# Kernel tuning notes

Measured on AMD Instinct MI355X. Metric: run time of the kernel, lower is better.

## Reference

```python
import jax, jax.numpy as jnp
import numpy as np

N_EMBED = 1024
HEAD_SIZE = 64
BLOCK_SIZE = 2048


def setup_inputs() -> dict:
    key = jax.random.key(0)
    kx, kk, kv = jax.random.split(key, 3)
    x = jax.random.normal(kx, (8, 2048, N_EMBED), dtype=jnp.float32)
    # nn.Linear(n_embed, head_size, bias=False): weight [head_size, n_embed]
    scale = 1.0 / np.sqrt(N_EMBED)
    W_k = jax.random.uniform(kk, (HEAD_SIZE, N_EMBED), dtype=jnp.float32, minval=-scale, maxval=scale)
    W_v = jax.random.uniform(kv, (HEAD_SIZE, N_EMBED), dtype=jnp.float32, minval=-scale, maxval=scale)
    return {"x": x, "W_k": W_k, "W_v": W_v}


def reference(x, W_k, W_v):
    # Faithful to source: q = self.key(x) (query projection is unused in the original forward)
    T = x.shape[1]
    k = jnp.einsum('btc,hc->bth', x, W_k)   # [B,T,H]
    q = k                                    # source bug: q uses key projection
    wei = jnp.einsum('bth,bsh->bts', q, k) * (HEAD_SIZE ** -0.5)  # [B,T,T]
    causal = jnp.tril(jnp.ones((T, T), dtype=bool))
    wei = jnp.where(causal, wei, -jnp.inf)
    wei = jax.nn.softmax(wei, axis=-1)
    v = jnp.einsum('btc,hc->bth', x, W_v)
    out = jnp.einsum('bts,bsh->bth', wei, v)
    return out
```

## Files before the change

kernel.cpp:

```cpp
#include <hip/hip_runtime.h>


typedef __bf16 bf16;
typedef __bf16 bf16x4 __attribute__((ext_vector_type(4)));
typedef __bf16 bf16x8 __attribute__((ext_vector_type(8)));
typedef float  floatx4 __attribute__((ext_vector_type(4)));

#define T_LEN 2048
#define HEAD  64
#define CEMB  1024

static __device__ __forceinline__ bf16x8 cvt2(float4 a, float4 b) {
    bf16x8 r;
    r[0] = (bf16)a.x; r[1] = (bf16)a.y; r[2] = (bf16)a.z; r[3] = (bf16)a.w;
    r[4] = (bf16)b.x; r[5] = (bf16)b.y; r[6] = (bf16)b.z; r[7] = (bf16)b.w;
    return r;
}

__global__ __launch_bounds__(256) void proj_kernel(const float* __restrict__ x,
                                                   const float* __restrict__ Wk,
                                                   const float* __restrict__ Wv,
                                                   bf16* __restrict__ Kbuf,
                                                   bf16* __restrict__ Vt) {
    __shared__ __align__(16) bf16 As[64][72];
    __shared__ __align__(16) bf16 Bs[128][72];

    const int tid  = threadIdx.x;
    const int wave = tid >> 6;
    const int lane = tid & 63;
    const int quad = lane >> 4;
    const int low  = lane & 15;

    const long row0 = (long)blockIdx.x * 64;

    const int a_row = tid >> 2;
    const int a_col = (tid & 3) * 16;
    const int b_row = tid >> 1;
    const int b_col = (tid & 1) * 32;

    const float* abase = x + (row0 + a_row) * CEMB + a_col;
    const float* wrow  = ((b_row < 64) ? (Wk + b_row * CEMB) : (Wv + (b_row - 64) * CEMB)) + b_col;

    floatx4 acc[8];
#pragma unroll
    for (int i = 0; i < 8; ++i) acc[i] = (floatx4){0.f, 0.f, 0.f, 0.f};

    float4 apf[4], bpf[8];
#pragma unroll
    for (int i = 0; i < 4; ++i) apf[i] = ((const float4*)abase)[i];
#pragma unroll
    for (int i = 0; i < 8; ++i) bpf[i] = ((const float4*)wrow)[i];

    for (int s = 0; s < 16; ++s) {
        __syncthreads();
        *(bf16x8*)&As[a_row][a_col]     = cvt2(apf[0], apf[1]);
        *(bf16x8*)&As[a_row][a_col + 8] = cvt2(apf[2], apf[3]);
#pragma unroll
        for (int i = 0; i < 4; ++i)
            *(bf16x8*)&Bs[b_row][b_col + 8 * i] = cvt2(bpf[2 * i], bpf[2 * i + 1]);

        if (s < 15) {
            const int k0 = (s + 1) * 64;
#pragma unroll
            for (int i = 0; i < 4; ++i) apf[i] = ((const float4*)(abase + k0))[i];
#pragma unroll
            for (int i = 0; i < 8; ++i) bpf[i] = ((const float4*)(wrow + k0))[i];
        }
        __syncthreads();

#pragma unroll
        for (int h = 0; h < 2; ++h) {
            bf16x8 afrag = *(const bf16x8*)&As[wave * 16 + low][h * 32 + quad * 8];
#pragma unroll
            for (int nt = 0; nt < 8; ++nt) {
                bf16x8 bfrag = *(const bf16x8*)&Bs[nt * 16 + low][h * 32 + quad * 8];
                acc[nt] = __builtin_amdgcn_mfma_f32_16x16x32_bf16(afrag, bfrag, acc[nt], 0, 0, 0);
            }
        }
    }

    const long b     = row0 >> 11;
    const int  tloc0 = (int)(row0 & 2047);
#pragma unroll
    for (int nt = 0; nt < 8; ++nt) {
#pragma unroll
        for (int r = 0; r < 4; ++r) {
            int trow = tloc0 + wave * 16 + quad * 4 + r;
            int c    = nt * 16 + low;
            bf16 val = (bf16)acc[nt][r];
            if (c < HEAD) {
                Kbuf[(b * T_LEN + trow) * HEAD + c] = val;
            } else {
                Vt[(b * HEAD + (c - HEAD)) * T_LEN + trow] = val;
            }
        }
    }
}

__global__ __launch_bounds__(256) void attn_kernel(const bf16* __restrict__ Kbuf,
                                                   const bf16* __restrict__ Vt,
                                                   float* __restrict__ out) {
    __shared__ __align__(16) bf16 Qs[64][72];
    __shared__ __align__(16) bf16 Ks[64][72];
    __shared__ __align__(16) bf16 Vs[64][72];
    __shared__ __align__(16) bf16 Ps[64][72];

    const int tid  = threadIdx.x;
    const int wave = tid >> 6;
    const int lane = tid & 63;
    const int quad = lane >> 4;
    const int low  = lane & 15;

    const int b  = blockIdx.x >> 5;
    const int qb = blockIdx.x & 31;

    const bf16* kbase = Kbuf + (long)b * T_LEN * HEAD;
    const bf16* vbase = Vt + (long)b * HEAD * T_LEN;

    const int s_row = tid >> 2;
    const int s_col = (tid & 3) * 16;

    {
        const bf16* src = kbase + (qb * 64 + s_row) * HEAD + s_col;
        *(float4*)&Qs[s_row][s_col]     = *(const float4*)(src);
        *(float4*)&Qs[s_row][s_col + 8] = *(const float4*)(src + 8);
    }
    __syncthreads();
    const bf16x8 qf0 = *(const bf16x8*)&Qs[wave * 16 + low][quad * 8];
    const bf16x8 qf1 = *(const bf16x8*)&Qs[wave * 16 + low][32 + quad * 8];

    bf16x8 ones;
#pragma unroll
    for (int i = 0; i < 8; ++i) ones[i] = (bf16)1.0f;

    floatx4 o[4], ol;
#pragma unroll
    for (int nt = 0; nt < 4; ++nt) o[nt] = (floatx4){0.f, 0.f, 0.f, 0.f};
    ol = (floatx4){0.f, 0.f, 0.f, 0.f};

    const bf16* ksrc = kbase + s_row * HEAD + s_col;
    const bf16* vsrc = vbase + (long)s_row * T_LEN + s_col;

    float4 kpf0 = *(const float4*)(ksrc);
    float4 kpf1 = *(const float4*)(ksrc + 8);
    float4 vpf0 = *(const float4*)(vsrc);
    float4 vpf1 = *(const float4*)(vsrc + 8);

    for (int j = 0; j <= qb; ++j) {
        __syncthreads();
        *(float4*)&Ks[s_row][s_col]     = kpf0;
        *(float4*)&Ks[s_row][s_col + 8] = kpf1;
        *(float4*)&Vs[s_row][s_col]     = vpf0;
        *(float4*)&Vs[s_row][s_col + 8] = vpf1;
        if (j < qb) {
            kpf0 = *(const float4*)(ksrc + (j + 1) * 4096);
            kpf1 = *(const float4*)(ksrc + (j + 1) * 4096 + 8);
            vpf0 = *(const float4*)(vsrc + (j + 1) * 64);
            vpf1 = *(const float4*)(vsrc + (j + 1) * 64 + 8);
        }
        __syncthreads();

        floatx4 s_[4];
#pragma unroll
        for (int nt = 0; nt < 4; ++nt) {
            bf16x8 kf0 = *(const bf16x8*)&Ks[nt * 16 + low][quad * 8];
            bf16x8 kf1 = *(const bf16x8*)&Ks[nt * 16 + low][32 + quad * 8];
            floatx4 z = (floatx4){0.f, 0.f, 0.f, 0.f};
            z = __builtin_amdgcn_mfma_f32_16x16x32_bf16(qf0, kf0, z, 0, 0, 0);
            z = __builtin_amdgcn_mfma_f32_16x16x32_bf16(qf1, kf1, z, 0, 0, 0);
            s_[nt] = z;
        }

        const bool diag = (j == qb);
#pragma unroll
        for (int nt = 0; nt < 4; ++nt) {
#pragma unroll
            for (int r = 0; r < 4; ++r) {
                float p = __builtin_amdgcn_exp2f(s_[nt][r] * 0.180336880f);
                if (diag && (nt * 16 + low) > (wave * 16 + quad * 4 + r)) p = 0.f;
                Ps[wave * 16 + quad * 4 + r][nt * 16 + low] = (bf16)p;
            }
        }

        bf16x8 pf0 = *(const bf16x8*)&Ps[wave * 16 + low][quad * 8];
        bf16x8 pf1 = *(const bf16x8*)&Ps[wave * 16 + low][32 + quad * 8];
#pragma unroll
        for (int nt = 0; nt < 4; ++nt) {
            bf16x8 vf0 = *(const bf16x8*)&Vs[nt * 16 + low][quad * 8];
            bf16x8 vf1 = *(const bf16x8*)&Vs[nt * 16 + low][32 + quad * 8];
            o[nt] = __builtin_amdgcn_mfma_f32_16x16x32_bf16(pf0, vf0, o[nt], 0, 0, 0);
            o[nt] = __builtin_amdgcn_mfma_f32_16x16x32_bf16(pf1, vf1, o[nt], 0, 0, 0);
        }
        ol = __builtin_amdgcn_mfma_f32_16x16x32_bf16(pf0, ones, ol, 0, 0, 0);
        ol = __builtin_amdgcn_mfma_f32_16x16x32_bf16(pf1, ones, ol, 0, 0, 0);
    }

#pragma unroll
    for (int nt = 0; nt < 4; ++nt) {
#pragma unroll
        for (int r = 0; r < 4; ++r) {
            int trow = qb * 64 + wave * 16 + quad * 4 + r;
            int h    = nt * 16 + low;
            out[((long)b * T_LEN + trow) * HEAD + h] = o[nt][r] / ol[r];
        }
    }
}

extern "C" void kernel_launch(void* const* d_in, const int* in_sizes, int n_in,
                              void* d_out, int out_size, void* d_ws, size_t ws_size,
                              hipStream_t stream) {
    const float* x  = (const float*)d_in[0];
    const float* Wk = (const float*)d_in[1];
    const float* Wv = (const float*)d_in[2];
    float* out = (float*)d_out;

    char* ws = (char*)d_ws;
    bf16* Kbuf = (bf16*)ws;
    bf16* Vt   = (bf16*)(ws + (2 << 20));

    proj_kernel<<<256, 256, 0, stream>>>(x, Wk, Wv, Kbuf, Vt);
    attn_kernel<<<256, 256, 0, stream>>>(Kbuf, Vt, out);
}
```

Baseline: 142.2 us.

## Split attention KV range across blocks and retile projection for more parallelism

The projection kernel now uses 32-row tiles, with each block computing either K or V, so it launches four times as many blocks. The attention kernel splits the causal KV loop of each query tile into four interleaved chunks, one per block, and writes unnormalized partial outputs and row sums to workspace. A new combine kernel sums the four partials and normalizes them. The aim is to fill the 256-CU device and reduce causal load imbalance, at the cost of an extra launch, partial-result traffic, and reloading the Q tile in every block.

```diff
diff --git a/kernel.cpp b/kernel.cpp
--- a/kernel.cpp
+++ b/kernel.cpp
@@ -2,7 +2,6 @@
 
 
 typedef __bf16 bf16;
-typedef __bf16 bf16x4 __attribute__((ext_vector_type(4)));
 typedef __bf16 bf16x8 __attribute__((ext_vector_type(8)));
 typedef float  floatx4 __attribute__((ext_vector_type(4)));
 
@@ -22,8 +21,8 @@
                                                    const float* __restrict__ Wv,
                                                    bf16* __restrict__ Kbuf,
                                                    bf16* __restrict__ Vt) {
-    __shared__ __align__(16) bf16 As[64][72];
-    __shared__ __align__(16) bf16 Bs[128][72];
+    __shared__ __align__(16) bf16 As[32][72];
+    __shared__ __align__(16) bf16 Bs[64][72];
 
     const int tid  = threadIdx.x;
     const int wave = tid >> 6;
@@ -31,75 +30,75 @@
     const int quad = lane >> 4;
     const int low  = lane & 15;
 
-    const long row0 = (long)blockIdx.x * 64;
-
-    const int a_row = tid >> 2;
-    const int a_col = (tid & 3) * 16;
-    const int b_row = tid >> 1;
-    const int b_col = (tid & 1) * 32;
+    const int mblk  = blockIdx.x >> 1;
+    const int nhalf = blockIdx.x & 1;
+    const long row0 = (long)mblk * 32;
+
+    const int a_row = tid >> 3;
+    const int a_col = (tid & 7) * 8;
+    const int b_row = tid >> 2;
+    const int b_col = (tid & 3) * 16;
 
     const float* abase = x + (row0 + a_row) * CEMB + a_col;
-    const float* wrow  = ((b_row < 64) ? (Wk + b_row * CEMB) : (Wv + (b_row - 64) * CEMB)) + b_col;
-
-    floatx4 acc[8];
-#pragma unroll
-    for (int i = 0; i < 8; ++i) acc[i] = (floatx4){0.f, 0.f, 0.f, 0.f};
-
-    float4 apf[4], bpf[8];
-#pragma unroll
-    for (int i = 0; i < 4; ++i) apf[i] = ((const float4*)abase)[i];
-#pragma unroll
-    for (int i = 0; i < 8; ++i) bpf[i] = ((const float4*)wrow)[i];
+    const float* wrow  = (nhalf ? Wv : Wk) + b_row * CEMB + b_col;
+
+    const int strip = wave & 1;
+    const int npair = wave >> 1;
+
+    floatx4 acc[2];
+    acc[0] = (floatx4){0.f, 0.f, 0.f, 0.f};
+    acc[1] = (floatx4){0.f, 0.f, 0.f, 0.f};
+
+    float4 apf[2], bpf[4];
+#pragma unroll
+    for (int i = 0; i < 2; ++i) apf[i] = ((const float4*)abase)[i];
+#pragma unroll
+    for (int i = 0; i < 4; ++i) bpf[i] = ((const float4*)wrow)[i];
 
     for (int s = 0; s < 16; ++s) {
         __syncthreads();
-        *(bf16x8*)&As[a_row][a_col]     = cvt2(apf[0], apf[1]);
-        *(bf16x8*)&As[a_row][a_col + 8] = cvt2(apf[2], apf[3]);
-#pragma unroll
-        for (int i = 0; i < 4; ++i)
-            *(bf16x8*)&Bs[b_row][b_col + 8 * i] = cvt2(bpf[2 * i], bpf[2 * i + 1]);
-
+        *(bf16x8*)&As[a_row][a_col] = cvt2(apf[0], apf[1]);
+        *(bf16x8*)&Bs[b_row][b_col]     = cvt2(bpf[0], bpf[1]);
+        *(bf16x8*)&Bs[b_row][b_col + 8] = cvt2(bpf[2], bpf[3]);
         if (s < 15) {
             const int k0 = (s + 1) * 64;
 #pragma unroll
-            for (int i = 0; i < 4; ++i) apf[i] = ((const float4*)(abase + k0))[i];
-#pragma unroll
-            for (int i = 0; i < 8; ++i) bpf[i] = ((const float4*)(wrow + k0))[i];
+            for (int i = 0; i < 2; ++i) apf[i] = ((const float4*)(abase + k0))[i];
+#pragma unroll
+            for (int i = 0; i < 4; ++i) bpf[i] = ((const float4*)(wrow + k0))[i];
         }
         __syncthreads();
 
 #pragma unroll
         for (int h = 0; h < 2; ++h) {
-            bf16x8 afrag = *(const bf16x8*)&As[wave * 16 + low][h * 32 + quad * 8];
-#pragma unroll
-            for (int nt = 0; nt < 8; ++nt) {
-                bf16x8 bfrag = *(const bf16x8*)&Bs[nt * 16 + low][h * 32 + quad * 8];
-                acc[nt] = __builtin_amdgcn_mfma_f32_16x16x32_bf16(afrag, bfrag, acc[nt], 0, 0, 0);
-            }
-        }
-    }
-
-    const long b     = row0 >> 11;
-    const int  tloc0 = (int)(row0 & 2047);
-#pragma unroll
-    for (int nt = 0; nt < 8; ++nt) {
+            bf16x8 afrag = *(const bf16x8*)&As[strip * 16 + low][h * 32 + quad * 8];
+#pragma unroll
+            for (int i = 0; i < 2; ++i) {
+                bf16x8 bfrag = *(const bf16x8*)&Bs[(npair * 2 + i) * 16 + low][h * 32 + quad * 8];
+                acc[i] = __builtin_amdgcn_mfma_f32_16x16x32_bf16(afrag, bfrag, acc[i], 0, 0, 0);
+            }
+        }
+    }
+
+#pragma unroll
+    for (int i = 0; i < 2; ++i) {
 #pragma unroll
         for (int r = 0; r < 4; ++r) {
-            int trow = tloc0 + wave * 16 + quad * 4 + r;
-            int c    = nt * 16 + low;
-            bf16 val = (bf16)acc[nt][r];
-            if (c < HEAD) {
-                Kbuf[(b * T_LEN + trow) * HEAD + c] = val;
-            } else {
-                Vt[(b * HEAD + (c - HEAD)) * T_LEN + trow] = val;
-            }
+            long trow = row0 + strip * 16 + quad * 4 + r;
+            long b    = trow >> 11;
+            int  tloc = (int)(trow & 2047);
+            int  cl   = (npair * 2 + i) * 16 + low;
+            bf16 val  = (bf16)acc[i][r];
+            if (nhalf == 0) Kbuf[(b * T_LEN + tloc) * HEAD + cl] = val;
+            else            Vt[(b * HEAD + cl) * T_LEN + tloc]   = val;
         }
     }
 }
 
 __global__ __launch_bounds__(256) void attn_kernel(const bf16* __restrict__ Kbuf,
                                                    const bf16* __restrict__ Vt,
-                                                   float* __restrict__ out) {
+                                                   float* __restrict__ Opart,
+                                                   float* __restrict__ lpart) {
     __shared__ __align__(16) bf16 Qs[64][72];
     __shared__ __align__(16) bf16 Ks[64][72];
     __shared__ __align__(16) bf16 Vs[64][72];
@@ -111,8 +110,9 @@
     const int quad = lane >> 4;
     const int low  = lane & 15;
 
-    const int b  = blockIdx.x >> 5;
-    const int qb = blockIdx.x & 31;
+    const int c  = blockIdx.x & 3;
+    const int qb = (blockIdx.x >> 2) & 31;
+    const int b  = blockIdx.x >> 7;
 
     const bf16* kbase = Kbuf + (long)b * T_LEN * HEAD;
     const bf16* vbase = Vt + (long)b * HEAD * T_LEN;
@@ -141,69 +141,109 @@
     const bf16* ksrc = kbase + s_row * HEAD + s_col;
     const bf16* vsrc = vbase + (long)s_row * T_LEN + s_col;
 
-    float4 kpf0 = *(const float4*)(ksrc);
-    float4 kpf1 = *(const float4*)(ksrc + 8);
-    float4 vpf0 = *(const float4*)(vsrc);
-    float4 vpf1 = *(const float4*)(vsrc + 8);
-
-    for (int j = 0; j <= qb; ++j) {
-        __syncthreads();
-        *(float4*)&Ks[s_row][s_col]     = kpf0;
-        *(float4*)&Ks[s_row][s_col + 8] = kpf1;
-        *(float4*)&Vs[s_row][s_col]     = vpf0;
-        *(float4*)&Vs[s_row][s_col + 8] = vpf1;
-        if (j < qb) {
-            kpf0 = *(const float4*)(ksrc + (j + 1) * 4096);
-            kpf1 = *(const float4*)(ksrc + (j + 1) * 4096 + 8);
-            vpf0 = *(const float4*)(vsrc + (j + 1) * 64);
-            vpf1 = *(const float4*)(vsrc + (j + 1) * 64 + 8);
-        }
-        __syncthreads();
-
-        floatx4 s_[4];
-#pragma unroll
-        for (int nt = 0; nt < 4; ++nt) {
-            bf16x8 kf0 = *(const bf16x8*)&Ks[nt * 16 + low][quad * 8];
-            bf16x8 kf1 = *(const bf16x8*)&Ks[nt * 16 + low][32 + quad * 8];
-            floatx4 z = (floatx4){0.f, 0.f, 0.f, 0.f};
-            z = __builtin_amdgcn_mfma_f32_16x16x32_bf16(qf0, kf0, z, 0, 0, 0);
-            z = __builtin_amdgcn_mfma_f32_16x16x32_bf16(qf1, kf1, z, 0, 0, 0);
-            s_[nt] = z;
-        }
-
-        const bool diag = (j == qb);
-#pragma unroll
-        for (int nt = 0; nt < 4; ++nt) {
-#pragma unroll
-            for (int r = 0; r < 4; ++r) {
-                float p = __builtin_amdgcn_exp2f(s_[nt][r] * 0.180336880f);
-                if (diag && (nt * 16 + low) > (wave * 16 + quad * 4 + r)) p = 0.f;
-                Ps[wave * 16 + quad * 4 + r][nt * 16 + low] = (bf16)p;
-            }
-        }
-
-        bf16x8 pf0 = *(const bf16x8*)&Ps[wave * 16 + low][quad * 8];
-        bf16x8 pf1 = *(const bf16x8*)&Ps[wave * 16 + low][32 + quad * 8];
-#pragma unroll
-        for (int nt = 0; nt < 4; ++nt) {
-            bf16x8 vf0 = *(const bf16x8*)&Vs[nt * 16 + low][quad * 8];
-            bf16x8 vf1 = *(const bf16x8*)&Vs[nt * 16 + low][32 + quad * 8];
-            o[nt] = __builtin_amdgcn_mfma_f32_16x16x32_bf16(pf0, vf0, o[nt], 0, 0, 0);
-            o[nt] = __builtin_amdgcn_mfma_f32_16x16x32_bf16(pf1, vf1, o[nt], 0, 0, 0);
-        }
-        ol = __builtin_amdgcn_mfma_f32_16x16x32_bf16(pf0, ones, ol, 0, 0, 0);
-        ol = __builtin_amdgcn_mfma_f32_16x16x32_bf16(pf1, ones, ol, 0, 0, 0);
-    }
-
+    if (c <= qb) {
+        float4 kpf0 = *(const float4*)(ksrc + c * 4096);
+        float4 kpf1 = *(const float4*)(ksrc + c * 4096 + 8);
+        float4 vpf0 = *(const float4*)(vsrc + c * 64);
+        float4 vpf1 = *(const float4*)(vsrc + c * 64 + 8);
+
+        for (int j = c; j <= qb; j += 4) {
+            __syncthreads();
+            *(float4*)&Ks[s_row][s_col]     = kpf0;
+            *(float4*)&Ks[s_row][s_col + 8] = kpf1;
+            *(float4*)&Vs[s_row][s_col]     = vpf0;
+            *(float4*)&Vs[s_row][s_col + 8] = vpf1;
+            if (j + 4 <= qb) {
+                kpf0 = *(const float4*)(ksrc + (j + 4) * 4096);
+                kpf1 = *(const float4*)(ksrc + (j + 4) * 4096 + 8);
+                vpf0 = *(const float4*)(vsrc + (j + 4) * 64);
+                vpf1 = *(const float4*)(vsrc + (j + 4) * 64 + 8);
+            }
+            __syncthreads();
+
+            floatx4 s_[4];
+#pragma unroll
+            for (int nt = 0; nt < 4; ++nt) {
+                bf16x8 kf0 = *(const bf16x8*)&Ks[nt * 16 + low][quad * 8];
+                bf16x8 kf1 = *(const bf16x8*)&Ks[nt * 16 + low][32 + quad * 8];
+                floatx4 z = (floatx4){0.f, 0.f, 0.f, 0.f};
+                z = __builtin_amdgcn_mfma_f32_16x16x32_bf16(qf0, kf0, z, 0, 0, 0);
+                z = __builtin_amdgcn_mfma_f32_16x16x32_bf16(qf1, kf1, z, 0, 0, 0);
+                s_[nt] = z;
+            }
+
+            const bool diag = (j == qb);
+#pragma unroll
+            for (int nt = 0; nt < 4; ++nt) {
+#pragma unroll
+                for (int r = 0; r < 4; ++r) {
+                    float p = __builtin_amdgcn_exp2f(s_[nt][r] * 0.180336880f);
+                    if (diag && (nt * 16 + low) > (wave * 16 + quad * 4 + r)) p = 0.f;
+                    Ps[wave * 16 + quad * 4 + r][nt * 16 + low] = (bf16)p;
+                }
+            }
+
+            bf16x8 pf0 = *(const bf16x8*)&Ps[wave * 16 + low][quad * 8];
+            bf16x8 pf1 = *(const bf16x8*)&Ps[wave * 16 + low][32 + quad * 8];
+#pragma unroll
+            for (int nt = 0; nt < 4; ++nt) {
+                bf16x8 vf0 = *(const bf16x8*)&Vs[nt * 16 + low][quad * 8];
+                bf16x8 vf1 = *(const bf16x8*)&Vs[nt * 16 + low][32 + quad * 8];
+                o[nt] = __builtin_amdgcn_mfma_f32_16x16x32_bf16(pf0, vf0, o[nt], 0, 0, 0);
+                o[nt] = __builtin_amdgcn_mfma_f32_16x16x32_bf16(pf1, vf1, o[nt], 0, 0, 0);
+            }
+            ol = __builtin_amdgcn_mfma_f32_16x16x32_bf16(pf0, ones, ol, 0, 0, 0);
+            ol = __builtin_amdgcn_mfma_f32_16x16x32_bf16(pf1, ones, ol, 0, 0, 0);
+        }
+    }
+
+    float* ob = Opart + (long)blockIdx.x * 4096;
 #pragma unroll
     for (int nt = 0; nt < 4; ++nt) {
 #pragma unroll
         for (int r = 0; r < 4; ++r) {
-            int trow = qb * 64 + wave * 16 + quad * 4 + r;
-            int h    = nt * 16 + low;
-            out[((long)b * T_LEN + trow) * HEAD + h] = o[nt][r] / ol[r];
-        }
-    }
+            int row = wave * 16 + quad * 4 + r;
+            ob[row * 64 + nt * 16 + low] = o[nt][r];
+        }
+    }
+    if (low == 0) {
+#pragma unroll
+        for (int r = 0; r < 4; ++r)
+            lpart[(long)blockIdx.x * 64 + wave * 16 + quad * 4 + r] = ol[r];
+    }
+}
+
+__global__ __launch_bounds__(256) void attn_combine(const float* __restrict__ Opart,
+                                                    const float* __restrict__ lpart,
+                                                    float* __restrict__ out) {
+    const int tile = blockIdx.x;
+    const int tid  = threadIdx.x;
+    const int row  = tid >> 2;
+    const int col0 = (tid & 3) * 16;
+
+    const float* ob = Opart + (long)tile * 4 * 4096 + row * 64 + col0;
+    const float* lb = lpart + (long)tile * 4 * 64 + row;
+
+    float l = lb[0] + lb[64] + lb[128] + lb[192];
+    float rl = 1.0f / l;
+
+    float4 s0 = (float4){0.f, 0.f, 0.f, 0.f}, s1 = s0, s2 = s0, s3 = s0;
+#pragma unroll
+    for (int ch = 0; ch < 4; ++ch) {
+        const float4* p = (const float4*)(ob + ch * 4096);
+        float4 a = p[0], b = p[1], c = p[2], d = p[3];
+        s0.x += a.x; s0.y += a.y; s0.z += a.z; s0.w += a.w;
+        s1.x += b.x; s1.y += b.y; s1.z += b.z; s1.w += b.w;
+        s2.x += c.x; s2.y += c.y; s2.z += c.z; s2.w += c.w;
+        s3.x += d.x; s3.y += d.y; s3.z += d.z; s3.w += d.w;
+    }
+    s0.x *= rl; s0.y *= rl; s0.z *= rl; s0.w *= rl;
+    s1.x *= rl; s1.y *= rl; s1.z *= rl; s1.w *= rl;
+    s2.x *= rl; s2.y *= rl; s2.z *= rl; s2.w *= rl;
+    s3.x *= rl; s3.y *= rl; s3.z *= rl; s3.w *= rl;
+
+    float4* op = (float4*)(out + (long)tile * 4096 + row * 64 + col0);
+    op[0] = s0; op[1] = s1; op[2] = s2; op[3] = s3;
 }
 
 extern "C" void kernel_launch(void* const* d_in, const int* in_sizes, int n_in,
@@ -215,9 +255,12 @@
     float* out = (float*)d_out;
 
     char* ws = (char*)d_ws;
-    bf16* Kbuf = (bf16*)ws;
-    bf16* Vt   = (bf16*)(ws + (2 << 20));
-
-    proj_kernel<<<256, 256, 0, stream>>>(x, Wk, Wv, Kbuf, Vt);
-    attn_kernel<<<256, 256, 0, stream>>>(Kbuf, Vt, out);
-}
+    bf16*  Kbuf  = (bf16*)ws;
+    bf16*  Vt    = (bf16*)(ws + (2 << 20));
+    float* Opart = (float*)(ws + (4 << 20));
+    float* lpart = (float*)(ws + (20 << 20));
+
+    proj_kernel<<<1024, 256, 0, stream>>>(x, Wk, Wv, Kbuf, Vt);
+    attn_kernel<<<1024, 256, 0, stream>>>(Kbuf, Vt, Opart, lpart);
+    attn_combine<<<256, 256, 0, stream>>>(Opart, lpart, out);
+}
```

Result: slower. 149.1 us (+4.9%).
